# Kernel tuning notes

Measured on AMD Instinct MI355X. Metric: run time of the kernel, lower is better.

The kernel has to match this reference:

```python
import jax, jax.numpy as jnp
import numpy as np

B, N, H = 16, 8192, 128
TOK_MLP, CH_MLP = 256, 512
EPS = 1e-5


def _layer_norm(z, g, b):
    m = jnp.mean(z, axis=-1, keepdims=True)
    v = jnp.mean(jnp.square(z - m), axis=-1, keepdims=True)
    return (z - m) * jax.lax.rsqrt(v + EPS) * g + b


def setup_inputs() -> dict:
    key = jax.random.key(0)
    ks = jax.random.split(key, 9)
    s = 0.02
    return {
        "x": jax.random.normal(ks[0], (B, N, H), dtype=jnp.float32),
        "ln1_g": jnp.ones((H,), jnp.float32),
        "ln1_b": jnp.zeros((H,), jnp.float32),
        "ln2_g": jnp.ones((H,), jnp.float32),
        "ln2_b": jnp.zeros((H,), jnp.float32),
        "tok_w1": jax.random.normal(ks[1], (N, TOK_MLP), jnp.float32) * s,
        "tok_b1": jnp.zeros((TOK_MLP,), jnp.float32),
        "tok_w2": jax.random.normal(ks[2], (TOK_MLP, N), jnp.float32) * s,
        "tok_b2": jnp.zeros((N,), jnp.float32),
        "ch_w1": jax.random.normal(ks[3], (H, CH_MLP), jnp.float32) * s,
        "ch_b1": jnp.zeros((CH_MLP,), jnp.float32),
        "ch_w2": jax.random.normal(ks[4], (CH_MLP, H), jnp.float32) * s,
        "ch_b2": jnp.zeros((H,), jnp.float32),
    }


def reference(x, ln1_g, ln1_b, ln2_g, ln2_b,
              tok_w1, tok_b1, tok_w2, tok_b2,
              ch_w1, ch_b1, ch_w2, ch_b2):
    # x: [B, N, H]
    y = _layer_norm(x, ln1_g, ln1_b)
    # mask-expand-multiply-sum over dim=2 == reverse (suffix) cumsum over tokens:
    # out[b, j, h] = sum_{i >= j} y[b, i, h]
    y = jnp.flip(jnp.cumsum(jnp.flip(y, axis=1), axis=1), axis=1)  # [B, N, H]
    y = jnp.swapaxes(y, 1, 2)                                      # [B, H, N]
    h = jax.nn.gelu(y @ tok_w1 + tok_b1, approximate=False)        # [B, H, TOK_MLP]
    y = h @ tok_w2 + tok_b2                                        # [B, H, N]
    y = jnp.swapaxes(y, 1, 2)                                      # [B, N, H]
    y = _layer_norm(y, ln2_g, ln2_b)
    h = jax.nn.gelu(y @ ch_w1 + ch_b1, approximate=False)          # [B, N, CH_MLP]
    return h @ ch_w2 + ch_b2                                       # [B, N, H]
```

## Files before the change

### kernel.cpp

```cpp
#include <hip/hip_runtime.h>
#include <math.h>

#define B_ 16
#define N_ 8192
#define H_ 128
#define T_ 256
#define C_ 512

typedef __bf16 bf16x8 __attribute__((ext_vector_type(8)));
typedef __bf16 bf16x4 __attribute__((ext_vector_type(4)));
typedef float f32x4 __attribute__((ext_vector_type(4)));

__device__ __forceinline__ float gelu_f(float x) {
    float p = fmaf(0.044715f * x * x, x, x);
    float e = __expf(-1.5957691216057308f * p);
    return x * __builtin_amdgcn_rcpf(1.f + e);
}

__device__ __forceinline__ unsigned short f2bf(float x) {
    unsigned int u = __float_as_uint(x);
    u = (u + 0x7FFFu + ((u >> 16) & 1u)) >> 16;
    return (unsigned short)u;
}

__device__ __forceinline__ void gl2lds16(const void* g, void* l) {
    __builtin_amdgcn_global_load_lds(
        (const __attribute__((address_space(1))) void*)g,
        (__attribute__((address_space(3))) void*)l,
        16, 0, 0);
}

__global__ void k_w1_psum(const float* __restrict__ w1, float* __restrict__ psum) {
    int c = blockIdx.x, t = threadIdx.x;
    const float* p = w1 + (size_t)c * 64 * T_ + t;
    float s = 0.f;
    #pragma unroll 8
    for (int r = 0; r < 64; ++r) s += p[(size_t)r * T_];
    psum[c * T_ + t] = s;
}

__global__ void k_w1_scan(const float* __restrict__ psum, float* __restrict__ offs) {
    int t = threadIdx.x;
    float run = 0.f;
    for (int c = 0; c < 128; ++c) {
        offs[c * T_ + t] = run;
        run += psum[c * T_ + t];
    }
}

__global__ void k_w1_prefix(const float* __restrict__ w1, const float* __restrict__ offs,
                            unsigned short* __restrict__ w1ct) {
    int c = blockIdx.x, t = threadIdx.x;
    float run = offs[c * T_ + t];
    const float* p = w1 + (size_t)c * 64 * T_ + t;
    unsigned int wb[32];
    #pragma unroll
    for (int q = 0; q < 32; ++q) {
        run += p[(size_t)(2 * q) * T_];
        unsigned int lo = f2bf(run);
        run += p[(size_t)(2 * q + 1) * T_];
        wb[q] = lo | ((unsigned int)f2bf(run) << 16);
    }
    char* row = (char*)w1ct + ((size_t)t * N_ + c * 64) * 2;
    int key = (t & 7) << 4;
    #pragma unroll
    for (int pc = 0; pc < 8; ++pc) {
        int4 v = { (int)wb[4*pc], (int)wb[4*pc+1], (int)wb[4*pc+2], (int)wb[4*pc+3] };
        *(int4*)(row + ((pc * 16) ^ key)) = v;
    }
}

__global__ void k_w2t_pack(const float* __restrict__ w2, unsigned short* __restrict__ w2t) {
    __shared__ float ld[64 * 68];
    int nt = blockIdx.x, tt = blockIdx.y;
    int n0 = nt * 64, t0 = tt * 64;
    int tid = threadIdx.x;
    #pragma unroll
    for (int rnd = 0; rnd < 4; ++rnd) {
        int idx = tid + rnd * 256;
        int tr = idx >> 4, nc = idx & 15;
        float4 v = *(const float4*)(w2 + (size_t)(t0 + tr) * N_ + n0 + nc * 4);
        *(float4*)&ld[tr * 68 + nc * 4] = v;
    }
    __syncthreads();
    int n = tid >> 2, q = tid & 3;
    int key = (n & 7) << 4;
    unsigned int wb[8];
    #pragma unroll
    for (int j = 0; j < 8; ++j) {
        float a = ld[(q * 16 + 2 * j) * 68 + n];
        float b = ld[(q * 16 + 2 * j + 1) * 68 + n];
        wb[j] = (unsigned int)f2bf(a) | ((unsigned int)f2bf(b) << 16);
    }
    char* row = (char*)w2t + (size_t)(n0 + n) * 512 + t0 * 2;
    int4 v0 = { (int)wb[0], (int)wb[1], (int)wb[2], (int)wb[3] };
    int4 v1 = { (int)wb[4], (int)wb[5], (int)wb[6], (int)wb[7] };
    *(int4*)(row + ((q * 32) ^ key)) = v0;
    *(int4*)(row + ((q * 32 + 16) ^ key)) = v1;
}

__global__ void k_packw(const float* __restrict__ w1, const float* __restrict__ w2,
                        unsigned short* __restrict__ w1p, unsigned short* __restrict__ w2p) {
    int e = blockIdx.x * 256 + threadIdx.x;
    if (blockIdx.y == 0) {
        int c = e >> 13, t = e & 8191;
        int n = t >> 7, j = t & 127;
        int k = j ^ ((n & 7) << 3);
        int hid = c * 64 + n;
        w1p[e] = f2bf(w1[(size_t)k * C_ + hid]);
    } else {
        int c = e >> 13, t = e & 8191;
        int n = t >> 6, j = t & 63;
        int k = j ^ ((n & 7) << 3);
        w2p[e] = f2bf(w2[(size_t)(c * 64 + k) * H_ + n]);
    }
}

__global__ void k_lnT(const float* __restrict__ x, const float* __restrict__ g,
                      const float* __restrict__ bb, unsigned short* __restrict__ y1t) {
    __shared__ float ln[64 * 129];
    int tid = threadIdx.x;
    int wave = tid >> 6, lane = tid & 63;
    size_t base = (size_t)blockIdx.x * 64;
    float2 gg = *(const float2*)(g + lane * 2);
    float2 bv = *(const float2*)(bb + lane * 2);
    for (int rr = 0; rr < 16; ++rr) {
        int r = wave * 16 + rr;
        float2 v = *(const float2*)(x + (base + r) * H_ + lane * 2);
        float s = v.x + v.y, ss = v.x * v.x + v.y * v.y;
        #pragma unroll
        for (int off = 32; off; off >>= 1) { s += __shfl_xor(s, off); ss += __shfl_xor(ss, off); }
        float mean = s * (1.f / 128.f);
        float rstd = rsqrtf(ss * (1.f / 128.f) - mean * mean + 1e-5f);
        ln[r * 129 + lane * 2]     = (v.x - mean) * rstd * gg.x + bv.x;
        ln[r * 129 + lane * 2 + 1] = (v.y - mean) * rstd * gg.y + bv.y;
    }
    __syncthreads();
    int h = tid >> 1, half = tid & 1;
    unsigned int wb[16];
    #pragma unroll
    for (int q = 0; q < 16; ++q) {
        float a = ln[(half * 32 + 2 * q) * 129 + h];
        float b = ln[(half * 32 + 2 * q + 1) * 129 + h];
        wb[q] = (unsigned int)f2bf(a) | ((unsigned int)f2bf(b) << 16);
    }
    int b_ = (int)(base >> 13);
    int n0 = (int)(base & (N_ - 1));
    char* row = (char*)y1t + (((size_t)b_ * H_ + h) * N_ + n0) * 2;
    int key = (h & 7) << 4;
    #pragma unroll
    for (int pc = 0; pc < 4; ++pc) {
        int4 v = { (int)wb[4*pc], (int)wb[4*pc+1], (int)wb[4*pc+2], (int)wb[4*pc+3] };
        *(int4*)(row + ((half * 64 + pc * 16) ^ key)) = v;
    }
}

#define T1_BUF 49152

__global__ __launch_bounds__(1024, 2)
void k_tok1(const unsigned short* __restrict__ y1t, const unsigned short* __restrict__ w1ct,
            float* __restrict__ P) {
    __shared__ __align__(16) char sm[98304];
    int kk = blockIdx.x, b = blockIdx.y;
    int tid = threadIdx.x;
    int w = tid >> 6, lane = tid & 63;
    int lr = lane & 15, lk = lane >> 4;
    int mg = w >> 2, ng = w & 3;
    const char* yb = (const char*)y1t + (size_t)b * H_ * N_ * 2;
    const char* wbg = (const char*)w1ct;
    int kbase = kk * 512;

    f32x4 acc[2][4];
    #pragma unroll
    for (int i = 0; i < 2; ++i)
        #pragma unroll
        for (int j = 0; j < 4; ++j) acc[i][j] = (f32x4){0.f, 0.f, 0.f, 0.f};

    {
        int hr = tid >> 3, p = tid & 7;
        gl2lds16(yb + ((size_t)hr * N_ + kbase) * 2 + p * 16, sm + tid * 16);
        #pragma unroll
        for (int rnd = 0; rnd < 2; ++rnd) {
            int idx = tid + rnd * 1024;
            int tr = idx >> 3, pp = idx & 7;
            gl2lds16(wbg + ((size_t)tr * N_ + kbase) * 2 + pp * 16, sm + 16384 + idx * 16);
        }
    }
    __syncthreads();

    for (int s = 0; s < 8; ++s) {
        const char* cur = sm + (s & 1) * T1_BUF;
        if (s < 7) {
            char* nxt = sm + ((s + 1) & 1) * T1_BUF;
            int n0 = kbase + (s + 1) * 64;
            int hr = tid >> 3, p = tid & 7;
            gl2lds16(yb + ((size_t)hr * N_ + n0) * 2 + p * 16, nxt + tid * 16);
            #pragma unroll
            for (int rnd = 0; rnd < 2; ++rnd) {
                int idx = tid + rnd * 1024;
                int tr = idx >> 3, pp = idx & 7;
                gl2lds16(wbg + ((size_t)tr * N_ + n0) * 2 + pp * 16, nxt + 16384 + idx * 16);
            }
        }
        #pragma unroll
        for (int ks = 0; ks < 2; ++ks) {
            bf16x8 af[2], bfr[4];
            #pragma unroll
            for (int i = 0; i < 2; ++i) {
                int h = mg * 32 + i * 16 + lr;
                af[i] = *(const bf16x8*)(cur + h * 128 + ((ks * 64 + lk * 16) ^ ((h & 7) << 4)));
            }
            #pragma unroll
            for (int j = 0; j < 4; ++j) {
                int t = ng * 64 + j * 16 + lr;
                bfr[j] = *(const bf16x8*)(cur + 16384 + t * 128 + ((ks * 64 + lk * 16) ^ ((t & 7) << 4)));
            }
            #pragma unroll
            for (int i = 0; i < 2; ++i)
                #pragma unroll
                for (int j = 0; j < 4; ++j)
                    acc[i][j] = __builtin_amdgcn_mfma_f32_16x16x32_bf16(af[i], bfr[j], acc[i][j], 0, 0, 0);
        }
        __syncthreads();
    }

    float* Pb = P + ((size_t)(b * 16 + kk)) * (H_ * T_);
    #pragma unroll
    for (int i = 0; i < 2; ++i)
        #pragma unroll
        for (int j = 0; j < 4; ++j) {
            int t = ng * 64 + j * 16 + lr;
            #pragma unroll
            for (int r = 0; r < 4; ++r) {
                int h = mg * 32 + i * 16 + lk * 4 + r;
                Pb[h * T_ + t] = acc[i][j][r];
            }
        }
}

__global__ void k_tok1_fin(const float* __restrict__ P, const float* __restrict__ b1,
                           unsigned short* __restrict__ g1b) {
    int fid = blockIdx.x * 256 + threadIdx.x;
    int base = fid * 4;
    int b = base >> 15, rem = base & 32767;
    int h = rem >> 8, t = rem & 255;
    const float* Pb = P + (size_t)b * 16 * 32768 + rem;
    float4 a = *(const float4*)Pb;
    #pragma unroll
    for (int kk = 1; kk < 16; ++kk) {
        float4 p = *(const float4*)(Pb + (size_t)kk * 32768);
        a.x += p.x; a.y += p.y; a.z += p.z; a.w += p.w;
    }
    float4 bb = *(const float4*)(b1 + t);
    unsigned int lo = (unsigned int)f2bf(gelu_f(a.x + bb.x)) | ((unsigned int)f2bf(gelu_f(a.y + bb.y)) << 16);
    unsigned int hi = (unsigned int)f2bf(gelu_f(a.z + bb.z)) | ((unsigned int)f2bf(gelu_f(a.w + bb.w)) << 16);
    char* row = (char*)g1b + (size_t)(b * H_ + h) * 512;
    uint2 v = { lo, hi };
    *(uint2*)(row + ((t * 2) ^ ((h & 7) << 4))) = v;
}

#define F_YS 0
#define F_HS 0
#define F_W2 32768
#define F_W1 49152

__global__ __launch_bounds__(512, 4)
void k_tok2mlp(const unsigned short* __restrict__ g1b, const unsigned short* __restrict__ w2t,
               const float* __restrict__ tb2, const float* __restrict__ lg,
               const float* __restrict__ lb, const unsigned short* __restrict__ w1p,
               const unsigned short* __restrict__ w2p, const float* __restrict__ b1g,
               const float* __restrict__ b2g, float* __restrict__ out) {
    __shared__ __align__(16) char sm[65536];
    int nt = blockIdx.x, b = blockIdx.y;
    int tid = threadIdx.x;
    int w = tid >> 6, lane = tid & 63;
    int lr = lane & 15, lk = lane >> 4;
    const char* ab = (const char*)w2t + (size_t)(nt * 128) * 512;
    const char* gb = (const char*)g1b + (size_t)b * H_ * 512;
    const char* w1b = (const char*)w1p;
    const char* w2b = (const char*)w2p;

    f32x4 acc[8];
    #pragma unroll
    for (int g = 0; g < 8; ++g) acc[g] = (f32x4){0.f, 0.f, 0.f, 0.f};

    int arow = w * 16 + lr;
    int akey = (arow & 7) << 4;

    #pragma unroll
    for (int rnd = 0; rnd < 2; ++rnd) {
        int idx = tid + rnd * 512;
        int row = idx >> 3, p = idx & 7;
        gl2lds16(ab + (size_t)row * 512 + p * 16, sm + row * 128 + p * 16);
        gl2lds16(gb + (size_t)row * 512 + p * 16, sm + 16384 + row * 128 + p * 16);
    }
    __syncthreads();

    for (int q = 0; q < 4; ++q) {
        const char* cur = sm + (q & 1) * 32768;
        if (q < 3) {
            char* nxt = sm + ((q + 1) & 1) * 32768;
            #pragma unroll
            for (int rnd = 0; rnd < 2; ++rnd) {
                int idx = tid + rnd * 512;
                int row = idx >> 3, p = idx & 7;
                gl2lds16(ab + (size_t)row * 512 + (q + 1) * 128 + p * 16, nxt + row * 128 + p * 16);
                gl2lds16(gb + (size_t)row * 512 + (q + 1) * 128 + p * 16, nxt + 16384 + row * 128 + p * 16);
            }
        }
        __builtin_amdgcn_s_setprio(1);
        #pragma unroll
        for (int ks = 0; ks < 2; ++ks) {
            bf16x8 af = *(const bf16x8*)(cur + arow * 128 + ((ks * 64 + lk * 16) ^ akey));
            #pragma unroll
            for (int g = 0; g < 8; ++g) {
                int hrow = g * 16 + lr;
                bf16x8 bf_ = *(const bf16x8*)(cur + 16384 + hrow * 128 + ((ks * 64 + lk * 16) ^ ((hrow & 7) << 4)));
                acc[g] = __builtin_amdgcn_mfma_f32_16x16x32_bf16(af, bf_, acc[g], 0, 0, 0);
            }
        }
        __builtin_amdgcn_s_setprio(0);
        __syncthreads();
    }

    float gam[8], bet[8];
    #pragma unroll
    for (int g = 0; g < 8; ++g) { gam[g] = lg[g * 16 + lr]; bet[g] = lb[g * 16 + lr]; }

    #pragma unroll
    for (int j = 0; j < 2; ++j) {
        gl2lds16(w1b + w * 2048 + j * 1024 + lane * 16, sm + F_W1 + w * 2048 + j * 1024);
        gl2lds16(w2b + w * 2048 + j * 1024 + lane * 16, sm + F_W2 + w * 2048 + j * 1024);
    }

    #pragma unroll
    for (int r = 0; r < 4; ++r) {
        int row = w * 16 + lk * 4 + r;
        float bias2 = tb2[nt * 128 + row];
        float vals[8];
        float s = 0.f, ss = 0.f;
        #pragma unroll
        for (int g = 0; g < 8; ++g) {
            float v = acc[g][r] + bias2;
            vals[g] = v; s += v; ss += v * v;
        }
        #pragma unroll
        for (int off = 8; off; off >>= 1) { s += __shfl_xor(s, off); ss += __shfl_xor(ss, off); }
        float mean = s * (1.f / 128.f);
        float rstd = rsqrtf(ss * (1.f / 128.f) - mean * mean + 1e-5f);
        int key = (row & 7) << 4;
        char* orow = sm + F_YS + row * 256;
        #pragma unroll
        for (int g = 0; g < 8; ++g) {
            float v = (vals[g] - mean) * rstd * gam[g] + bet[g];
            *(unsigned short*)(orow + (((g * 16 + lr) * 2) ^ key)) = f2bf(v);
        }
    }
    __syncthreads();

    int mg = w >> 1, ng = w & 1;
    int key = (lr & 7) << 4;

    bf16x8 yfrag[2][4];
    #pragma unroll
    for (int m = 0; m < 2; ++m) {
        int yrow = (2 * mg + m) * 16 + lr;
        #pragma unroll
        for (int kc = 0; kc < 4; ++kc)
            yfrag[m][kc] = *(const bf16x8*)(sm + F_YS + yrow * 256 + ((kc * 64 + lk * 16) ^ key));
    }
    __syncthreads();

    f32x4 oacc[2][4];
    #pragma unroll
    for (int m = 0; m < 2; ++m)
        #pragma unroll
        for (int n = 0; n < 4; ++n) oacc[m][n] = (f32x4){0.f, 0.f, 0.f, 0.f};

    for (int c = 0; c < 8; ++c) {
        f32x4 hacc[2][2];
        #pragma unroll
        for (int n = 0; n < 2; ++n) {
            float4 bv4 = *(const float4*)(b1g + c * 64 + (2 * ng + n) * 16 + lk * 4);
            f32x4 iv = { bv4.x, bv4.y, bv4.z, bv4.w };
            hacc[0][n] = iv;
            hacc[1][n] = iv;
        }
        __builtin_amdgcn_s_setprio(1);
        #pragma unroll
        for (int kc = 0; kc < 4; ++kc) {
            int ko = kc * 64 + lk * 16;
            bf16x8 b0 = *(const bf16x8*)(sm + F_W1 + ((2 * ng) * 16 + lr) * 256 + (ko ^ key));
            bf16x8 b1 = *(const bf16x8*)(sm + F_W1 + ((2 * ng + 1) * 16 + lr) * 256 + (ko ^ key));
            hacc[0][0] = __builtin_amdgcn_mfma_f32_16x16x32_bf16(b0, yfrag[0][kc], hacc[0][0], 0, 0, 0);
            hacc[0][1] = __builtin_amdgcn_mfma_f32_16x16x32_bf16(b1, yfrag[0][kc], hacc[0][1], 0, 0, 0);
            hacc[1][0] = __builtin_amdgcn_mfma_f32_16x16x32_bf16(b0, yfrag[1][kc], hacc[1][0], 0, 0, 0);
            hacc[1][1] = __builtin_amdgcn_mfma_f32_16x16x32_bf16(b1, yfrag[1][kc], hacc[1][1], 0, 0, 0);
        }
        __builtin_amdgcn_s_setprio(0);
        #pragma unroll
        for (int m = 0; m < 2; ++m)
            #pragma unroll
            for (int n = 0; n < 2; ++n) {
                int tok = (2 * mg + m) * 16 + lr;
                int hid0 = (2 * ng + n) * 16 + lk * 4;
                bf16x4 pv;
                pv[0] = (__bf16)gelu_f(hacc[m][n][0]);
                pv[1] = (__bf16)gelu_f(hacc[m][n][1]);
                pv[2] = (__bf16)gelu_f(hacc[m][n][2]);
                pv[3] = (__bf16)gelu_f(hacc[m][n][3]);
                *(bf16x4*)(sm + F_HS + tok * 128 + ((hid0 * 2) ^ ((tok & 7) << 4))) = pv;
            }
        __syncthreads();
        if (c < 7) {
            #pragma unroll
            for (int j = 0; j < 2; ++j)
                gl2lds16(w1b + (c + 1) * 16384 + w * 2048 + j * 1024 + lane * 16,
                         sm + F_W1 + w * 2048 + j * 1024);
        }
        __builtin_amdgcn_s_setprio(1);
        #pragma unroll
        for (int kc = 0; kc < 2; ++kc) {
            int ko = kc * 64 + lk * 16;
            int t0 = (2 * mg) * 16 + lr, t1 = (2 * mg + 1) * 16 + lr;
            bf16x8 a0 = *(const bf16x8*)(sm + F_HS + t0 * 128 + (ko ^ ((t0 & 7) << 4)));
            bf16x8 a1 = *(const bf16x8*)(sm + F_HS + t1 * 128 + (ko ^ ((t1 & 7) << 4)));
            #pragma unroll
            for (int n = 0; n < 4; ++n) {
                bf16x8 bb = *(const bf16x8*)(sm + F_W2 + ((ng * 4 + n) * 16 + lr) * 128 + (ko ^ key));
                oacc[0][n] = __builtin_amdgcn_mfma_f32_16x16x32_bf16(a0, bb, oacc[0][n], 0, 0, 0);
                oacc[1][n] = __builtin_amdgcn_mfma_f32_16x16x32_bf16(a1, bb, oacc[1][n], 0, 0, 0);
            }
        }
        __builtin_amdgcn_s_setprio(0);
        __syncthreads();
        if (c < 7) {
            #pragma unroll
            for (int j = 0; j < 2; ++j)
                gl2lds16(w2b + (c + 1) * 16384 + w * 2048 + j * 1024 + lane * 16,
                         sm + F_W2 + w * 2048 + j * 1024);
        }
    }

    size_t rbase = (size_t)(b * 64 + nt) * 128;
    #pragma unroll
    for (int n = 0; n < 4; ++n) {
        int ch = (ng * 4 + n) * 16 + lr;
        float bv = b2g[ch];
        #pragma unroll
        for (int m = 0; m < 2; ++m)
            #pragma unroll
            for (int r = 0; r < 4; ++r) {
                size_t row = rbase + (2 * mg + m) * 16 + lk * 4 + r;
                out[row * H_ + ch] = oacc[m][n][r] + bv;
            }
    }
}

extern "C" void kernel_launch(void* const* d_in, const int* in_sizes, int n_in,
                              void* d_out, int out_size, void* d_ws, size_t ws_size,
                              hipStream_t stream) {
    const float* x      = (const float*)d_in[0];
    const float* ln1_g  = (const float*)d_in[1];
    const float* ln1_b  = (const float*)d_in[2];
    const float* ln2_g  = (const float*)d_in[3];
    const float* ln2_b  = (const float*)d_in[4];
    const float* tok_w1 = (const float*)d_in[5];
    const float* tok_b1 = (const float*)d_in[6];
    const float* tok_w2 = (const float*)d_in[7];
    const float* tok_b2 = (const float*)d_in[8];
    const float* ch_w1  = (const float*)d_in[9];
    const float* ch_b1  = (const float*)d_in[10];
    const float* ch_w2  = (const float*)d_in[11];
    const float* ch_b2  = (const float*)d_in[12];
    float* out = (float*)d_out;
    float* ws  = (float*)d_ws;

    float* psum = ws;
    float* offs = ws + 32768;
    unsigned short* w1ct = (unsigned short*)(ws + 65536);
    unsigned short* w2t  = (unsigned short*)(ws + 1114112);
    unsigned short* w1p  = (unsigned short*)(ws + 2162688);
    unsigned short* w2p  = (unsigned short*)(ws + 2195456);
    unsigned short* y1t  = (unsigned short*)(ws + 2228224);
    unsigned short* g1b  = (unsigned short*)(ws + 10616832);
    float* P             = ws + 10878976;

    k_w1_psum<<<dim3(128), dim3(256), 0, stream>>>(tok_w1, psum);
    k_w1_scan<<<dim3(1), dim3(256), 0, stream>>>(psum, offs);
    k_w1_prefix<<<dim3(128), dim3(256), 0, stream>>>(tok_w1, offs, w1ct);
    k_w2t_pack<<<dim3(128, 4), dim3(256), 0, stream>>>(tok_w2, w2t);
    k_packw<<<dim3(256, 2), dim3(256), 0, stream>>>(ch_w1, ch_w2, w1p, w2p);
    k_lnT<<<dim3((B_ * N_) / 64), dim3(256), 0, stream>>>(x, ln1_g, ln1_b, y1t);
    k_tok1<<<dim3(16, 16), dim3(1024), 0, stream>>>(y1t, w1ct, P);
    k_tok1_fin<<<dim3(512), dim3(256), 0, stream>>>(P, tok_b1, g1b);
    k_tok2mlp<<<dim3(64, 16), dim3(512), 0, stream>>>(g1b, w2t, tok_b2, ln2_g, ln2_b,
                                                      w1p, w2p, ch_b1, ch_b2, out);
}
```

Measured before the change: 132.9 us.

## Merge weight-pack kernels, split tok1 over T halves, retile channel MLP

Folds the two weight-packing kernels into a single launch. k_tok1 now gives each block half of the T outputs over a K range twice as long, which halves LDS per block and the number of partial sums reduced in k_tok1_fin. The channel-MLP first GEMM is retiled so each wave holds four token fragments and loads one W1 fragment, cutting LDS reads of W1. The cost is more register pressure from the larger yfrag array and a longer serial K loop per block in tok1.

```diff
diff --git a/kernel.cpp b/kernel.cpp
--- a/kernel.cpp
+++ b/kernel.cpp
@@ -70,49 +70,51 @@
     }
 }
 
-__global__ void k_w2t_pack(const float* __restrict__ w2, unsigned short* __restrict__ w2t) {
+__global__ void k_packs(const float* __restrict__ w2, unsigned short* __restrict__ w2t,
+                        const float* __restrict__ cw1, const float* __restrict__ cw2,
+                        unsigned short* __restrict__ w1p, unsigned short* __restrict__ w2p) {
     __shared__ float ld[64 * 68];
-    int nt = blockIdx.x, tt = blockIdx.y;
-    int n0 = nt * 64, t0 = tt * 64;
     int tid = threadIdx.x;
-    #pragma unroll
-    for (int rnd = 0; rnd < 4; ++rnd) {
-        int idx = tid + rnd * 256;
-        int tr = idx >> 4, nc = idx & 15;
-        float4 v = *(const float4*)(w2 + (size_t)(t0 + tr) * N_ + n0 + nc * 4);
-        *(float4*)&ld[tr * 68 + nc * 4] = v;
-    }
-    __syncthreads();
-    int n = tid >> 2, q = tid & 3;
-    int key = (n & 7) << 4;
-    unsigned int wb[8];
-    #pragma unroll
-    for (int j = 0; j < 8; ++j) {
-        float a = ld[(q * 16 + 2 * j) * 68 + n];
-        float b = ld[(q * 16 + 2 * j + 1) * 68 + n];
-        wb[j] = (unsigned int)f2bf(a) | ((unsigned int)f2bf(b) << 16);
-    }
-    char* row = (char*)w2t + (size_t)(n0 + n) * 512 + t0 * 2;
-    int4 v0 = { (int)wb[0], (int)wb[1], (int)wb[2], (int)wb[3] };
-    int4 v1 = { (int)wb[4], (int)wb[5], (int)wb[6], (int)wb[7] };
-    *(int4*)(row + ((q * 32) ^ key)) = v0;
-    *(int4*)(row + ((q * 32 + 16) ^ key)) = v1;
-}
-
-__global__ void k_packw(const float* __restrict__ w1, const float* __restrict__ w2,
-                        unsigned short* __restrict__ w1p, unsigned short* __restrict__ w2p) {
-    int e = blockIdx.x * 256 + threadIdx.x;
-    if (blockIdx.y == 0) {
-        int c = e >> 13, t = e & 8191;
-        int n = t >> 7, j = t & 127;
-        int k = j ^ ((n & 7) << 3);
-        int hid = c * 64 + n;
-        w1p[e] = f2bf(w1[(size_t)k * C_ + hid]);
+    if (blockIdx.y < 4) {
+        int nt = blockIdx.x, tt = blockIdx.y;
+        int n0 = nt * 64, t0 = tt * 64;
+        #pragma unroll
+        for (int rnd = 0; rnd < 4; ++rnd) {
+            int idx = tid + rnd * 256;
+            int tr = idx >> 4, nc = idx & 15;
+            float4 v = *(const float4*)(w2 + (size_t)(t0 + tr) * N_ + n0 + nc * 4);
+            *(float4*)&ld[tr * 68 + nc * 4] = v;
+        }
+        __syncthreads();
+        int n = tid >> 2, q = tid & 3;
+        int key = (n & 7) << 4;
+        unsigned int wb[8];
+        #pragma unroll
+        for (int j = 0; j < 8; ++j) {
+            float a = ld[(q * 16 + 2 * j) * 68 + n];
+            float b = ld[(q * 16 + 2 * j + 1) * 68 + n];
+            wb[j] = (unsigned int)f2bf(a) | ((unsigned int)f2bf(b) << 16);
+        }
+        char* row = (char*)w2t + (size_t)(n0 + n) * 512 + t0 * 2;
+        int4 v0 = { (int)wb[0], (int)wb[1], (int)wb[2], (int)wb[3] };
+        int4 v1 = { (int)wb[4], (int)wb[5], (int)wb[6], (int)wb[7] };
+        *(int4*)(row + ((q * 32) ^ key)) = v0;
+        *(int4*)(row + ((q * 32 + 16) ^ key)) = v1;
     } else {
-        int c = e >> 13, t = e & 8191;
-        int n = t >> 6, j = t & 63;
-        int k = j ^ ((n & 7) << 3);
-        w2p[e] = f2bf(w2[(size_t)(c * 64 + k) * H_ + n]);
+        int e = ((blockIdx.y - 4) * 128 + blockIdx.x) * 256 + tid;
+        if (e < 65536) {
+            int c = e >> 13, t = e & 8191;
+            int n = t >> 7, j = t & 127;
+            int k = j ^ ((n & 7) << 3);
+            int hid = c * 64 + n;
+            w1p[e] = f2bf(cw1[(size_t)k * C_ + hid]);
+        } else {
+            int e2 = e - 65536;
+            int c = e2 >> 13, t = e2 & 8191;
+            int n = t >> 6, j = t & 63;
+            int k = j ^ ((n & 7) << 3);
+            w2p[e2] = f2bf(cw2[(size_t)(c * 64 + k) * H_ + n]);
+        }
     }
 }
 
@@ -155,84 +157,74 @@
     }
 }
 
-#define T1_BUF 49152
+#define T1_BUF 32768
 
 __global__ __launch_bounds__(1024, 2)
 void k_tok1(const unsigned short* __restrict__ y1t, const unsigned short* __restrict__ w1ct,
             float* __restrict__ P) {
-    __shared__ __align__(16) char sm[98304];
-    int kk = blockIdx.x, b = blockIdx.y;
+    __shared__ __align__(16) char sm[65536];
+    int kk = blockIdx.x >> 1, tt = blockIdx.x & 1, b = blockIdx.y;
     int tid = threadIdx.x;
     int w = tid >> 6, lane = tid & 63;
     int lr = lane & 15, lk = lane >> 4;
-    int mg = w >> 2, ng = w & 3;
+    int hg = w >> 2, tg = w & 3;
     const char* yb = (const char*)y1t + (size_t)b * H_ * N_ * 2;
-    const char* wbg = (const char*)w1ct;
-    int kbase = kk * 512;
-
-    f32x4 acc[2][4];
+    const char* wbg = (const char*)w1ct + (size_t)(tt * 128) * N_ * 2;
+    int kbase = kk * 1024;
+
+    f32x4 acc[2][2];
     #pragma unroll
     for (int i = 0; i < 2; ++i)
         #pragma unroll
-        for (int j = 0; j < 4; ++j) acc[i][j] = (f32x4){0.f, 0.f, 0.f, 0.f};
+        for (int j = 0; j < 2; ++j) acc[i][j] = (f32x4){0.f, 0.f, 0.f, 0.f};
 
     {
-        int hr = tid >> 3, p = tid & 7;
-        gl2lds16(yb + ((size_t)hr * N_ + kbase) * 2 + p * 16, sm + tid * 16);
-        #pragma unroll
-        for (int rnd = 0; rnd < 2; ++rnd) {
-            int idx = tid + rnd * 1024;
-            int tr = idx >> 3, pp = idx & 7;
-            gl2lds16(wbg + ((size_t)tr * N_ + kbase) * 2 + pp * 16, sm + 16384 + idx * 16);
-        }
+        int row = tid >> 3, p = tid & 7;
+        gl2lds16(yb + ((size_t)row * N_ + kbase) * 2 + p * 16, sm + tid * 16);
+        gl2lds16(wbg + ((size_t)row * N_ + kbase) * 2 + p * 16, sm + 16384 + tid * 16);
     }
     __syncthreads();
 
-    for (int s = 0; s < 8; ++s) {
+    for (int s = 0; s < 16; ++s) {
         const char* cur = sm + (s & 1) * T1_BUF;
-        if (s < 7) {
+        if (s < 15) {
             char* nxt = sm + ((s + 1) & 1) * T1_BUF;
             int n0 = kbase + (s + 1) * 64;
-            int hr = tid >> 3, p = tid & 7;
-            gl2lds16(yb + ((size_t)hr * N_ + n0) * 2 + p * 16, nxt + tid * 16);
-            #pragma unroll
-            for (int rnd = 0; rnd < 2; ++rnd) {
-                int idx = tid + rnd * 1024;
-                int tr = idx >> 3, pp = idx & 7;
-                gl2lds16(wbg + ((size_t)tr * N_ + n0) * 2 + pp * 16, nxt + 16384 + idx * 16);
-            }
+            int row = tid >> 3, p = tid & 7;
+            gl2lds16(yb + ((size_t)row * N_ + n0) * 2 + p * 16, nxt + tid * 16);
+            gl2lds16(wbg + ((size_t)row * N_ + n0) * 2 + p * 16, nxt + 16384 + tid * 16);
         }
         #pragma unroll
         for (int ks = 0; ks < 2; ++ks) {
-            bf16x8 af[2], bfr[4];
+            bf16x8 af[2], bfr[2];
             #pragma unroll
             for (int i = 0; i < 2; ++i) {
-                int h = mg * 32 + i * 16 + lr;
+                int h = hg * 32 + i * 16 + lr;
                 af[i] = *(const bf16x8*)(cur + h * 128 + ((ks * 64 + lk * 16) ^ ((h & 7) << 4)));
             }
             #pragma unroll
-            for (int j = 0; j < 4; ++j) {
-                int t = ng * 64 + j * 16 + lr;
+            for (int j = 0; j < 2; ++j) {
+                int t = tg * 32 + j * 16 + lr;
                 bfr[j] = *(const bf16x8*)(cur + 16384 + t * 128 + ((ks * 64 + lk * 16) ^ ((t & 7) << 4)));
             }
             #pragma unroll
             for (int i = 0; i < 2; ++i)
                 #pragma unroll
-                for (int j = 0; j < 4; ++j)
+                for (int j = 0; j < 2; ++j)
                     acc[i][j] = __builtin_amdgcn_mfma_f32_16x16x32_bf16(af[i], bfr[j], acc[i][j], 0, 0, 0);
         }
         __syncthreads();
     }
 
-    float* Pb = P + ((size_t)(b * 16 + kk)) * (H_ * T_);
+    float* Pb = P + (size_t)(b * 8 + kk) * (H_ * T_);
     #pragma unroll
     for (int i = 0; i < 2; ++i)
         #pragma unroll
-        for (int j = 0; j < 4; ++j) {
-            int t = ng * 64 + j * 16 + lr;
+        for (int j = 0; j < 2; ++j) {
+            int t = tt * 128 + tg * 32 + j * 16 + lr;
             #pragma unroll
             for (int r = 0; r < 4; ++r) {
-                int h = mg * 32 + i * 16 + lk * 4 + r;
+                int h = hg * 32 + i * 16 + lk * 4 + r;
                 Pb[h * T_ + t] = acc[i][j][r];
             }
         }
@@ -244,10 +236,10 @@
     int base = fid * 4;
     int b = base >> 15, rem = base & 32767;
     int h = rem >> 8, t = rem & 255;
-    const float* Pb = P + (size_t)b * 16 * 32768 + rem;
+    const float* Pb = P + (size_t)b * 8 * 32768 + rem;
     float4 a = *(const float4*)Pb;
     #pragma unroll
-    for (int kk = 1; kk < 16; ++kk) {
+    for (int kk = 1; kk < 8; ++kk) {
         float4 p = *(const float4*)(Pb + (size_t)kk * 32768);
         a.x += p.x; a.y += p.y; a.z += p.z; a.w += p.w;
     }
@@ -358,13 +350,14 @@
     }
     __syncthreads();
 
+    int mga = w >> 2, nga = w & 3;
     int mg = w >> 1, ng = w & 1;
     int key = (lr & 7) << 4;
 
-    bf16x8 yfrag[2][4];
-    #pragma unroll
-    for (int m = 0; m < 2; ++m) {
-        int yrow = (2 * mg + m) * 16 + lr;
+    bf16x8 yfrag[4][4];
+    #pragma unroll
+    for (int m = 0; m < 4; ++m) {
+        int yrow = mga * 64 + m * 16 + lr;
         #pragma unroll
         for (int kc = 0; kc < 4; ++kc)
             yfrag[m][kc] = *(const bf16x8*)(sm + F_YS + yrow * 256 + ((kc * 64 + lk * 16) ^ key));
@@ -378,39 +371,34 @@
         for (int n = 0; n < 4; ++n) oacc[m][n] = (f32x4){0.f, 0.f, 0.f, 0.f};
 
     for (int c = 0; c < 8; ++c) {
-        f32x4 hacc[2][2];
-        #pragma unroll
-        for (int n = 0; n < 2; ++n) {
-            float4 bv4 = *(const float4*)(b1g + c * 64 + (2 * ng + n) * 16 + lk * 4);
+        f32x4 hacc[4];
+        {
+            float4 bv4 = *(const float4*)(b1g + c * 64 + nga * 16 + lk * 4);
             f32x4 iv = { bv4.x, bv4.y, bv4.z, bv4.w };
-            hacc[0][n] = iv;
-            hacc[1][n] = iv;
+            #pragma unroll
+            for (int m = 0; m < 4; ++m) hacc[m] = iv;
         }
         __builtin_amdgcn_s_setprio(1);
         #pragma unroll
         for (int kc = 0; kc < 4; ++kc) {
             int ko = kc * 64 + lk * 16;
-            bf16x8 b0 = *(const bf16x8*)(sm + F_W1 + ((2 * ng) * 16 + lr) * 256 + (ko ^ key));
-            bf16x8 b1 = *(const bf16x8*)(sm + F_W1 + ((2 * ng + 1) * 16 + lr) * 256 + (ko ^ key));
-            hacc[0][0] = __builtin_amdgcn_mfma_f32_16x16x32_bf16(b0, yfrag[0][kc], hacc[0][0], 0, 0, 0);
-            hacc[0][1] = __builtin_amdgcn_mfma_f32_16x16x32_bf16(b1, yfrag[0][kc], hacc[0][1], 0, 0, 0);
-            hacc[1][0] = __builtin_amdgcn_mfma_f32_16x16x32_bf16(b0, yfrag[1][kc], hacc[1][0], 0, 0, 0);
-            hacc[1][1] = __builtin_amdgcn_mfma_f32_16x16x32_bf16(b1, yfrag[1][kc], hacc[1][1], 0, 0, 0);
+            bf16x8 b0 = *(const bf16x8*)(sm + F_W1 + (nga * 16 + lr) * 256 + (ko ^ key));
+            #pragma unroll
+            for (int m = 0; m < 4; ++m)
+                hacc[m] = __builtin_amdgcn_mfma_f32_16x16x32_bf16(b0, yfrag[m][kc], hacc[m], 0, 0, 0);
         }
         __builtin_amdgcn_s_setprio(0);
         #pragma unroll
-        for (int m = 0; m < 2; ++m)
-            #pragma unroll
-            for (int n = 0; n < 2; ++n) {
-                int tok = (2 * mg + m) * 16 + lr;
-                int hid0 = (2 * ng + n) * 16 + lk * 4;
-                bf16x4 pv;
-                pv[0] = (__bf16)gelu_f(hacc[m][n][0]);
-                pv[1] = (__bf16)gelu_f(hacc[m][n][1]);
-                pv[2] = (__bf16)gelu_f(hacc[m][n][2]);
-                pv[3] = (__bf16)gelu_f(hacc[m][n][3]);
-                *(bf16x4*)(sm + F_HS + tok * 128 + ((hid0 * 2) ^ ((tok & 7) << 4))) = pv;
-            }
+        for (int m = 0; m < 4; ++m) {
+            int tok = mga * 64 + m * 16 + lr;
+            int hid0 = nga * 16 + lk * 4;
+            bf16x4 pv;
+            pv[0] = (__bf16)gelu_f(hacc[m][0]);
+            pv[1] = (__bf16)gelu_f(hacc[m][1]);
+            pv[2] = (__bf16)gelu_f(hacc[m][2]);
+            pv[3] = (__bf16)gelu_f(hacc[m][3]);
+            *(bf16x4*)(sm + F_HS + tok * 128 + ((hid0 * 2) ^ ((tok & 7) << 4))) = pv;
+        }
         __syncthreads();
         if (c < 7) {
             #pragma unroll
@@ -489,8 +477,7 @@
     k_w1_psum<<<dim3(128), dim3(256), 0, stream>>>(tok_w1, psum);
     k_w1_scan<<<dim3(1), dim3(256), 0, stream>>>(psum, offs);
     k_w1_prefix<<<dim3(128), dim3(256), 0, stream>>>(tok_w1, offs, w1ct);
-    k_w2t_pack<<<dim3(128, 4), dim3(256), 0, stream>>>(tok_w2, w2t);
-    k_packw<<<dim3(256, 2), dim3(256), 0, stream>>>(ch_w1, ch_w2, w1p, w2p);
+    k_packs<<<dim3(128, 8), dim3(256), 0, stream>>>(tok_w2, w2t, ch_w1, ch_w2, w1p, w2p);
     k_lnT<<<dim3((B_ * N_) / 64), dim3(256), 0, stream>>>(x, ln1_g, ln1_b, y1t);
     k_tok1<<<dim3(16, 16), dim3(1024), 0, stream>>>(y1t, w1ct, P);
     k_tok1_fin<<<dim3(512), dim3(256), 0, stream>>>(P, tok_b1, g1b);
```

Result: slower. 169.1 us (+27.2%).
